# Optimization experiments

Measured on AMD Instinct MI355X. Metric: run time of the kernel, lower is better.

Reference implementation:

```python
import math
import jax, jax.numpy as jnp
import numpy as np

N_HEAD = 16
STEP_DIM = 4


def _make_mask(T):
    # lower-triangular causal mask with every STEP_DIM-th column zeroed
    m = jnp.tril(jnp.ones((T, T), dtype=jnp.float32))
    cols = jnp.arange(T)
    keep_col = (cols % STEP_DIM) != (STEP_DIM - 1)
    return m * keep_col[None, :].astype(jnp.float32)  # [T, T]


def setup_inputs() -> dict:
    key = jax.random.key(0)
    ks = jax.random.split(key, 9)
    B, T, C = 2, 2048, 1024
    s = 1.0 / math.sqrt(C)
    return {
        "x": jax.random.normal(ks[0], (B, T, C), dtype=jnp.float32),
        "Wq": jax.random.normal(ks[1], (C, C), dtype=jnp.float32) * s,
        "bq": jnp.zeros((C,), dtype=jnp.float32),
        "Wk": jax.random.normal(ks[2], (C, C), dtype=jnp.float32) * s,
        "bk": jnp.zeros((C,), dtype=jnp.float32),
        "Wv": jax.random.normal(ks[3], (C, C), dtype=jnp.float32) * s,
        "bv": jnp.zeros((C,), dtype=jnp.float32),
        "Wp": jax.random.normal(ks[4], (C, C), dtype=jnp.float32) * s,
        "bp": jnp.zeros((C,), dtype=jnp.float32),
    }


def reference(x, Wq, bq, Wk, bk, Wv, bv, Wp, bp):
    B, T, C = x.shape
    H = N_HEAD
    D = C // H
    # QKV projections -> [B, H, T, D]
    def heads(y):
        return y.reshape(B, T, H, D).transpose(0, 2, 1, 3)
    q = heads(x @ Wq + bq)
    k = heads(x @ Wk + bk)
    v = heads(x @ Wv + bv)
    # scores [B, H, T, T]
    att = jnp.einsum("bhtd,bhsd->bhts", q, k) * (1.0 / math.sqrt(D))
    mask = _make_mask(T)  # [T, T]
    att = jnp.where(mask[None, None, :, :] == 0, -jnp.inf, att)
    att = jax.nn.softmax(att, axis=-1)
    y = jnp.einsum("bhts,bhsd->bhtd", att, v)  # [B, H, T, D]
    y = y.transpose(0, 2, 1, 3).reshape(B, T, C)
    return y @ Wp + bp
```

## Files before the change

### kernel.cpp

```cpp
#include <hip/hip_runtime.h>

typedef __bf16 bf16x8 __attribute__((ext_vector_type(8)));
typedef float  f32x4  __attribute__((ext_vector_type(4)));
typedef unsigned int u32x2 __attribute__((ext_vector_type(2)));
typedef unsigned short u16x8 __attribute__((ext_vector_type(8)));
typedef __attribute__((address_space(3))) const unsigned short* lds_cp;

#define T_SEQ 2048
#define C_DIM 1024
#define NH    16
#define HD    64
#define LOG2E 1.4426950408889634f

__device__ __forceinline__ unsigned short f2bf(float f) {
  unsigned u = __builtin_bit_cast(unsigned, f);
  u += 0x7FFFu + ((u >> 16) & 1u);
  return (unsigned short)(u >> 16);
}

__device__ __forceinline__ unsigned cvtpk(float lo, float hi) {
  unsigned r;
  asm("v_cvt_pk_bf16_f32 %0, %1, %2" : "=v"(r) : "v"(lo), "v"(hi));
  return r;
}

__device__ __forceinline__ bf16x8 tr_frag(lds_cp addr) {
  u32x2 lo, hi;
  asm volatile("ds_read_b64_tr_b16 %0, %2 offset:0\n\t"
               "ds_read_b64_tr_b16 %1, %2 offset:128"
               : "=&v"(lo), "=&v"(hi) : "v"(addr) : "memory");
  struct { u32x2 a, b; } s{lo, hi};
  return __builtin_bit_cast(bf16x8, s);
}

__device__ __forceinline__ void gload_lds16(const void* g, void* l) {
  __builtin_amdgcn_global_load_lds(
      (const __attribute__((address_space(1))) unsigned int*)g,
      (__attribute__((address_space(3))) unsigned int*)l, 16, 0, 0);
}

__global__ void k_cvt_x(const float* __restrict__ x, unsigned short* __restrict__ xb) {
  const int i = blockIdx.x * 256 + threadIdx.x;
  const float4 v = ((const float4*)x)[i];
  ushort4 o;
  o.x = f2bf(v.x); o.y = f2bf(v.y); o.z = f2bf(v.z); o.w = f2bf(v.w);
  ((ushort4*)xb)[i] = o;
}

__global__ void k_transpose_w(const float* __restrict__ W, unsigned short* __restrict__ Wt) {
  __shared__ float tile[32][33];
  const int tx = threadIdx.x, ty = threadIdx.y;
  const int n0 = blockIdx.x * 32, k0 = blockIdx.y * 32;
#pragma unroll
  for (int i = 0; i < 32; i += 8)
    tile[ty + i][tx] = W[(size_t)(k0 + ty + i) * C_DIM + n0 + tx];
  __syncthreads();
#pragma unroll
  for (int i = 0; i < 32; i += 8)
    Wt[(size_t)(n0 + ty + i) * C_DIM + k0 + tx] = f2bf(tile[tx][ty + i]);
}

__global__ void k_concat_bias(const float* __restrict__ bq, const float* __restrict__ bk,
                              const float* __restrict__ bv, float* __restrict__ o) {
  const int i = blockIdx.x * 256 + threadIdx.x;
  o[i] = (i < 1024) ? bq[i] : (i < 2048 ? bk[i - 1024] : bv[i - 2048]);
}

template<int KDIM>
__device__ __forceinline__ void gemm_tile_mainloop(
    const unsigned short* __restrict__ A,
    const unsigned short* __restrict__ Bt,
    int m0, int n0,
    unsigned short* As, unsigned short* Bs,
    f32x4 acc[4][4])
{
  const int tid  = threadIdx.x;
  const int lane = tid & 63;
  const int wave = tid >> 6;
  const int wr   = wave >> 1, wc = wave & 1;
  const int srow = lane >> 2;
  const int scol = (lane & 3) << 3;
  const int fr   = lane & 15, g = lane >> 4;

  const f32x4 zero = {0.f, 0.f, 0.f, 0.f};
#pragma unroll
  for (int m = 0; m < 4; ++m)
#pragma unroll
    for (int n = 0; n < 4; ++n) acc[m][n] = zero;

  const int nk = KDIM >> 5;
  for (int kt = 0; kt < nk; ++kt) {
    const int kb = kt << 5;
#pragma unroll
    for (int i = 0; i < 2; ++i) {
      const int c   = wave * 2 + i;
      const int row = c * 16 + srow;
      gload_lds16(A  + (size_t)(m0 + row) * KDIM + kb + scol, As + c * 512);
      gload_lds16(Bt + (size_t)(n0 + row) * KDIM + kb + scol, Bs + c * 512);
    }
    __syncthreads();
    bf16x8 af[4], bfr[4];
    const unsigned short* ap = As + (wr * 64 + fr) * 32 + g * 8;
    const unsigned short* bp = Bs + (wc * 64 + fr) * 32 + g * 8;
#pragma unroll
    for (int m = 0; m < 4; ++m) af[m]  = *(const bf16x8*)(ap + m * 512);
#pragma unroll
    for (int n = 0; n < 4; ++n) bfr[n] = *(const bf16x8*)(bp + n * 512);
#pragma unroll
    for (int m = 0; m < 4; ++m)
#pragma unroll
      for (int n = 0; n < 4; ++n)
        acc[m][n] = __builtin_amdgcn_mfma_f32_16x16x32_bf16(af[m], bfr[n], acc[m][n], 0, 0, 0);
    __syncthreads();
  }
}

__global__ __launch_bounds__(256) void k_gemm_qkv(
    const unsigned short* __restrict__ Xb,
    const unsigned short* __restrict__ Wt,
    const float* __restrict__ bias,
    unsigned short* __restrict__ Qb,
    unsigned short* __restrict__ Kb,
    unsigned short* __restrict__ Vt)
{
  __shared__ __attribute__((aligned(16))) unsigned short As[128 * 32];
  __shared__ __attribute__((aligned(16))) unsigned short Bs[128 * 32];
  f32x4 acc[4][4];
  const int m0 = blockIdx.y * 128, n0 = blockIdx.x * 128;
  gemm_tile_mainloop<1024>(Xb, Wt, m0, n0, As, Bs, acc);

  const int lane = threadIdx.x & 63, wave = threadIdx.x >> 6;
  const int wr = wave >> 1, wc = wave & 1;
  const int fr = lane & 15, g = lane >> 4;
  const int j = n0 >> 10;
#pragma unroll
  for (int ni = 0; ni < 4; ++ni) {
    const int col = n0 + wc * 64 + ni * 16 + fr;
    const int c = col & 1023, h = c >> 6, d = c & 63;
    const float bb = bias[col];
#pragma unroll
    for (int mi = 0; mi < 4; ++mi)
#pragma unroll
      for (int r = 0; r < 4; ++r) {
        const int row = m0 + wr * 64 + mi * 16 + g * 4 + r;
        const int b = row >> 11, t = row & 2047;
        const int bh = b * NH + h;
        const float v = acc[mi][ni][r] + bb;
        if (j == 0)      Qb[((size_t)bh * T_SEQ + t) * HD + d] = f2bf(v * (0.125f * LOG2E));
        else if (j == 1) Kb[((size_t)bh * T_SEQ + t) * HD + d] = f2bf(v);
        else             Vt[((size_t)bh * HD + d) * T_SEQ + t] =
                           ((t & 3) == 3) ? (unsigned short)0 : f2bf(v);
      }
  }
}

__global__ __launch_bounds__(128) void k_attn(
    const unsigned short* __restrict__ Qb,
    const unsigned short* __restrict__ Kb,
    const unsigned short* __restrict__ Vt,
    unsigned short* __restrict__ Yb)
{
  __shared__ __attribute__((aligned(128))) unsigned short Ks[2][64][64];
  __shared__ __attribute__((aligned(128))) unsigned short Vs[2][64][64];
  __shared__ __attribute__((aligned(128))) unsigned short Pc[2][2][64][16];

  const int i    = blockIdx.x;
  const int xcd  = i & 7;
  const int jj   = i >> 3;
  const int bh   = xcd * 4 + (jj & 3);
  const int qtile = 31 - (jj >> 2);
  const int lane  = threadIdx.x & 63;
  const int wave  = threadIdx.x >> 6;
  const int fr = lane & 15, g = lane >> 4;
  const int q0w = qtile * 64 + wave * 32;
  const int nt = qtile + 1;
  const size_t hbase = (size_t)bh * T_SEQ * HD;
  const unsigned short* Kh = Kb + hbase;
  const unsigned short* Vh = Vt + (size_t)bh * HD * T_SEQ;

  const int srow = lane >> 3;
  const int scol = ((lane & 7) ^ srow) << 3;
  const int frx  = (fr & 7) << 3;

  const unsigned short* qp = Qb + hbase + (size_t)(q0w + fr) * HD + g * 8;
  const bf16x8 qA0 = *(const bf16x8*)(qp);
  const bf16x8 qA1 = *(const bf16x8*)(qp + 32);
  const bf16x8 qB0 = *(const bf16x8*)(qp + 16 * HD);
  const bf16x8 qB1 = *(const bf16x8*)(qp + 16 * HD + 32);

  const u16x8 bo = {0x3F80u, 0x3F80u, 0x3F80u, 0u, 0x3F80u, 0x3F80u, 0x3F80u, 0u};
  const bf16x8 bones = __builtin_bit_cast(bf16x8, bo);

  const f32x4 zero = {0.f, 0.f, 0.f, 0.f};
  f32x4 yA[4], yB[4], lAcc, lBcc;
#pragma unroll
  for (int n = 0; n < 4; ++n) { yA[n] = zero; yB[n] = zero; }
  lAcc = zero; lBcc = zero;

  char* pwA = (char*)&Pc[wave][0][0][0] + fr * 32 + g * 8;
  char* pwB = (char*)&Pc[wave][1][0][0] + fr * 32 + g * 8;
  lds_cp trA = (lds_cp)(const unsigned short*)&Pc[wave][0][0][0] + fr * 4 + g * 128;
  lds_cp trB = (lds_cp)(const unsigned short*)&Pc[wave][1][0][0] + fr * 4 + g * 128;

  auto STAGE = [&](int buf, int s0) {
#pragma unroll
    for (int i2 = 0; i2 < 4; ++i2) {
      const int c = wave * 4 + i2;
      gload_lds16(Kh + (size_t)(s0 + c * 8 + srow) * HD + scol, &Ks[buf][c * 8][0]);
      gload_lds16(Vh + (size_t)(c * 8 + srow) * T_SEQ + s0 + scol, &Vs[buf][c * 8][0]);
    }
  };

  auto BODY = [&](int cur, int s0, bool diag) {
    bf16x8 kf[4][2];
#pragma unroll
    for (int n = 0; n < 4; ++n) {
      const unsigned short* kr = &Ks[cur][n * 16 + fr][0];
      kf[n][0] = *(const bf16x8*)(kr + ((g * 8) ^ frx));
      kf[n][1] = *(const bf16x8*)(kr + ((32 + g * 8) ^ frx));
    }
    f32x4 sA[4], sB[4];
#pragma unroll
    for (int n = 0; n < 4; ++n) {
      f32x4 a = zero, b = zero;
      a = __builtin_amdgcn_mfma_f32_16x16x32_bf16(qA0, kf[n][0], a, 0, 0, 0);
      a = __builtin_amdgcn_mfma_f32_16x16x32_bf16(qA1, kf[n][1], a, 0, 0, 0);
      b = __builtin_amdgcn_mfma_f32_16x16x32_bf16(qB0, kf[n][0], b, 0, 0, 0);
      b = __builtin_amdgcn_mfma_f32_16x16x32_bf16(qB1, kf[n][1], b, 0, 0, 0);
      sA[n] = a; sB[n] = b;
    }
    if (diag) {
#pragma unroll
      for (int n = 0; n < 4; ++n) {
        const int sc = s0 + n * 16 + fr;
#pragma unroll
        for (int r = 0; r < 4; ++r) {
          const int tA = q0w + g * 4 + r;
          sA[n][r] = (sc <= tA) ? sA[n][r] : -1e30f;
          sB[n][r] = (sc <= tA + 16) ? sB[n][r] : -1e30f;
        }
      }
    }
    bf16x8 vf[4][2];
#pragma unroll
    for (int n = 0; n < 4; ++n) {
      const unsigned short* vr = &Vs[cur][n * 16 + fr][0];
      vf[n][0] = *(const bf16x8*)(vr + ((g * 8) ^ frx));
      vf[n][1] = *(const bf16x8*)(vr + ((32 + g * 8) ^ frx));
    }
#pragma unroll
    for (int n = 0; n < 4; ++n) {
      u32x2 wa = {cvtpk(exp2f(sA[n][0]), exp2f(sA[n][1])),
                  cvtpk(exp2f(sA[n][2]), exp2f(sA[n][3]))};
      u32x2 wb = {cvtpk(exp2f(sB[n][0]), exp2f(sB[n][1])),
                  cvtpk(exp2f(sB[n][2]), exp2f(sB[n][3]))};
      *(u32x2*)(pwA + n * 512) = wa;
      *(u32x2*)(pwB + n * 512) = wb;
    }
    bf16x8 paA[2], paB[2];
    paA[0] = tr_frag(trA);       paA[1] = tr_frag(trA + 512);
    paB[0] = tr_frag(trB);       paB[1] = tr_frag(trB + 512);
    asm volatile("s_waitcnt lgkmcnt(0)" ::: "memory");
    __builtin_amdgcn_sched_barrier(0);
#pragma unroll
    for (int kk = 0; kk < 2; ++kk) {
#pragma unroll
      for (int n = 0; n < 4; ++n) {
        yA[n] = __builtin_amdgcn_mfma_f32_16x16x32_bf16(paA[kk], vf[n][kk], yA[n], 0, 0, 0);
        yB[n] = __builtin_amdgcn_mfma_f32_16x16x32_bf16(paB[kk], vf[n][kk], yB[n], 0, 0, 0);
      }
      lAcc = __builtin_amdgcn_mfma_f32_16x16x32_bf16(paA[kk], bones, lAcc, 0, 0, 0);
      lBcc = __builtin_amdgcn_mfma_f32_16x16x32_bf16(paB[kk], bones, lBcc, 0, 0, 0);
    }
  };

  STAGE(0, 0);
  __syncthreads();
  for (int t = 0; t < nt; ++t) {
    const int cur = t & 1;
    if (t + 1 < nt) STAGE(cur ^ 1, (t + 1) * 64);
    const int s0 = t * 64;
    BODY(cur, s0, s0 + 63 > q0w);
    __syncthreads();
  }

  const int b = bh >> 4, h = bh & 15;
#pragma unroll
  for (int r = 0; r < 4; ++r) {
    const float invA = 1.0f / lAcc[r], invB = 1.0f / lBcc[r];
    const int tA = q0w + g * 4 + r;
#pragma unroll
    for (int n = 0; n < 4; ++n) {
      Yb[((size_t)(b * T_SEQ + tA)) * C_DIM + h * HD + n * 16 + fr] = f2bf(yA[n][r] * invA);
      Yb[((size_t)(b * T_SEQ + tA + 16)) * C_DIM + h * HD + n * 16 + fr] = f2bf(yB[n][r] * invB);
    }
  }
}

__global__ __launch_bounds__(256) void k_gemm_out(
    const unsigned short* __restrict__ Yb,
    const unsigned short* __restrict__ Wpt,
    const float* __restrict__ bp,
    float* __restrict__ out)
{
  __shared__ __attribute__((aligned(16))) unsigned short As[128 * 32];
  __shared__ __attribute__((aligned(16))) unsigned short Bs[128 * 32];
  f32x4 acc[4][4];
  const int m0 = blockIdx.y * 128, n0 = blockIdx.x * 128;
  gemm_tile_mainloop<1024>(Yb, Wpt, m0, n0, As, Bs, acc);

  const int lane = threadIdx.x & 63, wave = threadIdx.x >> 6;
  const int wr = wave >> 1, wc = wave & 1;
  const int fr = lane & 15, g = lane >> 4;
#pragma unroll
  for (int ni = 0; ni < 4; ++ni) {
    const int col = n0 + wc * 64 + ni * 16 + fr;
    const float bb = bp[col];
#pragma unroll
    for (int mi = 0; mi < 4; ++mi)
#pragma unroll
      for (int r = 0; r < 4; ++r) {
        const int row = m0 + wr * 64 + mi * 16 + g * 4 + r;
        out[(size_t)row * C_DIM + col] = acc[mi][ni][r] + bb;
      }
  }
}

extern "C" void kernel_launch(void* const* d_in, const int* in_sizes, int n_in,
                              void* d_out, int out_size, void* d_ws, size_t ws_size,
                              hipStream_t stream) {
  const float* x  = (const float*)d_in[0];
  const float* Wq = (const float*)d_in[1];
  const float* bq = (const float*)d_in[2];
  const float* Wk = (const float*)d_in[3];
  const float* bk = (const float*)d_in[4];
  const float* Wv = (const float*)d_in[5];
  const float* bv = (const float*)d_in[6];
  const float* Wp = (const float*)d_in[7];
  const float* bp = (const float*)d_in[8];
  float* out = (float*)d_out;

  char* ws = (char*)d_ws;
  unsigned short* Xb   = (unsigned short*)(ws);
  unsigned short* Wt   = (unsigned short*)(ws + (8u  << 20));
  unsigned short* Wpt  = (unsigned short*)(ws + (14u << 20));
  float*          bqkv = (float*)         (ws + (16u << 20));
  unsigned short* Qb   = (unsigned short*)(ws + (16u << 20) + (64u << 10));
  unsigned short* Kb   = (unsigned short*)(ws + (24u << 20) + (64u << 10));
  unsigned short* Vt   = (unsigned short*)(ws + (32u << 20) + (64u << 10));
  unsigned short* Yb   = (unsigned short*)(ws + (40u << 20) + (64u << 10));

  k_cvt_x<<<4096, 256, 0, stream>>>(x, Xb);
  dim3 tb(32, 8);
  k_transpose_w<<<dim3(32, 32), tb, 0, stream>>>(Wq, Wt);
  k_transpose_w<<<dim3(32, 32), tb, 0, stream>>>(Wk, Wt + (1u << 20));
  k_transpose_w<<<dim3(32, 32), tb, 0, stream>>>(Wv, Wt + (2u << 20));
  k_transpose_w<<<dim3(32, 32), tb, 0, stream>>>(Wp, Wpt);
  k_concat_bias<<<12, 256, 0, stream>>>(bq, bk, bv, bqkv);
  k_gemm_qkv<<<dim3(24, 32), 256, 0, stream>>>(Xb, Wt, bqkv, Qb, Kb, Vt);
  k_attn<<<dim3(1024), 128, 0, stream>>>(Qb, Kb, Vt, Yb);
  k_gemm_out<<<dim3(8, 32), 256, 0, stream>>>(Yb, Wpt, bp, out);
}
```

Baseline: 144.6 us.

## Merge prep launches and add XCD-aware block mapping for GEMMs and attention

After: 130.9 us. -9.5%, faster.

```diff
diff --git a/kernel.cpp b/kernel.cpp
--- a/kernel.cpp
+++ b/kernel.cpp
@@ -39,16 +39,30 @@
       (__attribute__((address_space(3))) unsigned int*)l, 16, 0, 0);
 }
 
-__global__ void k_cvt_x(const float* __restrict__ x, unsigned short* __restrict__ xb) {
-  const int i = blockIdx.x * 256 + threadIdx.x;
-  const float4 v = ((const float4*)x)[i];
-  ushort4 o;
-  o.x = f2bf(v.x); o.y = f2bf(v.y); o.z = f2bf(v.z); o.w = f2bf(v.w);
-  ((ushort4*)xb)[i] = o;
-}
-
-__global__ void k_transpose_w(const float* __restrict__ W, unsigned short* __restrict__ Wt) {
+__global__ void k_cvt_x(const float* __restrict__ x, unsigned short* __restrict__ xb,
+                        const float* __restrict__ bq, const float* __restrict__ bk,
+                        const float* __restrict__ bv, float* __restrict__ bqkv) {
+  const int bx = blockIdx.x;
+  if (bx < 4096) {
+    const int i = bx * 256 + threadIdx.x;
+    const float4 v = ((const float4*)x)[i];
+    ushort4 o;
+    o.x = f2bf(v.x); o.y = f2bf(v.y); o.z = f2bf(v.z); o.w = f2bf(v.w);
+    ((ushort4*)xb)[i] = o;
+  } else {
+    const int i = (bx - 4096) * 256 + threadIdx.x;
+    bqkv[i] = (i < 1024) ? bq[i] : (i < 2048 ? bk[i - 1024] : bv[i - 2048]);
+  }
+}
+
+__global__ void k_transpose_w(const float* __restrict__ Wq, const float* __restrict__ Wk,
+                              const float* __restrict__ Wv, const float* __restrict__ Wp,
+                              unsigned short* __restrict__ Wt,
+                              unsigned short* __restrict__ Wpt) {
   __shared__ float tile[32][33];
+  const int z = blockIdx.z;
+  const float* W = (z == 0) ? Wq : (z == 1) ? Wk : (z == 2) ? Wv : Wp;
+  unsigned short* D = (z < 3) ? (Wt + ((size_t)z << 20)) : Wpt;
   const int tx = threadIdx.x, ty = threadIdx.y;
   const int n0 = blockIdx.x * 32, k0 = blockIdx.y * 32;
 #pragma unroll
@@ -57,13 +71,7 @@
   __syncthreads();
 #pragma unroll
   for (int i = 0; i < 32; i += 8)
-    Wt[(size_t)(n0 + ty + i) * C_DIM + k0 + tx] = f2bf(tile[tx][ty + i]);
-}
-
-__global__ void k_concat_bias(const float* __restrict__ bq, const float* __restrict__ bk,
-                              const float* __restrict__ bv, float* __restrict__ o) {
-  const int i = blockIdx.x * 256 + threadIdx.x;
-  o[i] = (i < 1024) ? bq[i] : (i < 2048 ? bk[i - 1024] : bv[i - 2048]);
+    D[(size_t)(n0 + ty + i) * C_DIM + k0 + tx] = f2bf(tile[tx][ty + i]);
 }
 
 template<int KDIM>
@@ -126,7 +134,11 @@
   __shared__ __attribute__((aligned(16))) unsigned short As[128 * 32];
   __shared__ __attribute__((aligned(16))) unsigned short Bs[128 * 32];
   f32x4 acc[4][4];
-  const int m0 = blockIdx.y * 128, n0 = blockIdx.x * 128;
+  const int bx  = blockIdx.x;
+  const int xcd = bx & 7;
+  const int jb  = bx >> 3;
+  const int m0  = (xcd * 4 + (jb & 3)) * 128;
+  const int n0  = (jb >> 2) * 128;
   gemm_tile_mainloop<1024>(Xb, Wt, m0, n0, As, Bs, acc);
 
   const int lane = threadIdx.x & 63, wave = threadIdx.x >> 6;
@@ -168,7 +180,10 @@
   const int xcd  = i & 7;
   const int jj   = i >> 3;
   const int bh   = xcd * 4 + (jj & 3);
-  const int qtile = 31 - (jj >> 2);
+  const int qs   = jj >> 2;
+  const int so   = qs >> 3;
+  const int qtile = (so == 0) ? 31 - qs : (so == 1) ? qs - 8
+                  : (so == 2) ? 39 - qs : qs - 16;
   const int lane  = threadIdx.x & 63;
   const int wave  = threadIdx.x >> 6;
   const int fr = lane & 15, g = lane >> 4;
@@ -306,7 +321,11 @@
   __shared__ __attribute__((aligned(16))) unsigned short As[128 * 32];
   __shared__ __attribute__((aligned(16))) unsigned short Bs[128 * 32];
   f32x4 acc[4][4];
-  const int m0 = blockIdx.y * 128, n0 = blockIdx.x * 128;
+  const int bx  = blockIdx.x;
+  const int xcd = bx & 7;
+  const int jb  = bx >> 3;
+  const int m0  = (xcd * 4 + (jb & 3)) * 128;
+  const int n0  = (jb >> 2) * 128;
   gemm_tile_mainloop<1024>(Yb, Wpt, m0, n0, As, Bs, acc);
 
   const int lane = threadIdx.x & 63, wave = threadIdx.x >> 6;
@@ -350,14 +369,10 @@
   unsigned short* Vt   = (unsigned short*)(ws + (32u << 20) + (64u << 10));
   unsigned short* Yb   = (unsigned short*)(ws + (40u << 20) + (64u << 10));
 
-  k_cvt_x<<<4096, 256, 0, stream>>>(x, Xb);
+  k_cvt_x<<<4108, 256, 0, stream>>>(x, Xb, bq, bk, bv, bqkv);
   dim3 tb(32, 8);
-  k_transpose_w<<<dim3(32, 32), tb, 0, stream>>>(Wq, Wt);
-  k_transpose_w<<<dim3(32, 32), tb, 0, stream>>>(Wk, Wt + (1u << 20));
-  k_transpose_w<<<dim3(32, 32), tb, 0, stream>>>(Wv, Wt + (2u << 20));
-  k_transpose_w<<<dim3(32, 32), tb, 0, stream>>>(Wp, Wpt);
-  k_concat_bias<<<12, 256, 0, stream>>>(bq, bk, bv, bqkv);
-  k_gemm_qkv<<<dim3(24, 32), 256, 0, stream>>>(Xb, Wt, bqkv, Qb, Kb, Vt);
+  k_transpose_w<<<dim3(32, 32, 4), tb, 0, stream>>>(Wq, Wk, Wv, Wp, Wt, Wpt);
+  k_gemm_qkv<<<dim3(768), 256, 0, stream>>>(Xb, Wt, bqkv, Qb, Kb, Vt);
   k_attn<<<dim3(1024), 128, 0, stream>>>(Qb, Kb, Vt, Yb);
-  k_gemm_out<<<dim3(8, 32), 256, 0, stream>>>(Yb, Wpt, bp, out);
-}
+  k_gemm_out<<<dim3(256), 256, 0, stream>>>(Yb, Wpt, bp, out);
+}
```
